# Optimization experiments

Hardware: AMD Instinct MI355X
Metric: run time of the kernel (lower is better)

Reference implementation:

```python
import jax, jax.numpy as jnp
import numpy as np

HEADS = 16
HEAD_DIM = 64
DIM = 1024
INNER = HEADS * HEAD_DIM
EPS = 1e-5


def setup_inputs() -> dict:
    key = jax.random.key(0)
    k_x, k_qkv, k_out, k_b = jax.random.split(key, 4)
    B, L = 2, 2048
    x = jax.random.normal(k_x, (B, L, DIM), dtype=jnp.float32)
    # Linear weights stored as [in, out] for x @ W
    w_qkv = jax.random.normal(k_qkv, (DIM, 3 * INNER), dtype=jnp.float32) * (DIM ** -0.5)
    w_out = jax.random.normal(k_out, (INNER, DIM), dtype=jnp.float32) * (INNER ** -0.5)
    b_out = jax.random.normal(k_b, (DIM,), dtype=jnp.float32) * 0.02
    gamma = jnp.ones((DIM,), dtype=jnp.float32)
    beta = jnp.zeros((DIM,), dtype=jnp.float32)
    return {"x": x, "w_qkv": w_qkv, "w_out": w_out, "b_out": b_out, "gamma": gamma, "beta": beta}


def reference(x, w_qkv, w_out, b_out, gamma, beta):
    B, L, C = x.shape
    scale = HEAD_DIM ** -0.5
    qkv = x @ w_qkv  # [B, L, 3*INNER]
    q, k, v = jnp.split(qkv, 3, axis=-1)
    # [B, L, INNER] -> [B, H, L, D]
    def split_heads(t):
        return t.reshape(B, L, HEADS, HEAD_DIM).transpose(0, 2, 1, 3)
    q, k, v = split_heads(q), split_heads(k), split_heads(v)
    dots = jnp.einsum('bhid,bhjd->bhij', q, k) * scale
    attn = jax.nn.softmax(dots, axis=-1)
    out = jnp.einsum('bhij,bhjd->bhid', attn, v)
    out = out.transpose(0, 2, 1, 3).reshape(B, L, INNER)
    out = out @ w_out + b_out
    res = x + out
    mean = jnp.mean(res, axis=-1, keepdims=True)
    var = jnp.var(res, axis=-1, keepdims=True)
    return (res - mean) * jax.lax.rsqrt(var + EPS) * gamma + beta
```

## Files before the change

kernel.cpp:

```cpp
#include <hip/hip_runtime.h>
#include <hip/hip_bf16.h>
#include <stdint.h>

#define HEADS 16
#define HDIM  64
#define DIMC  1024
#define INNER 1024
#define LSEQ  2048
#define BLM   4096

typedef unsigned short u16;
typedef __attribute__((ext_vector_type(8))) short bf16x8;
typedef __attribute__((ext_vector_type(4))) float f32x4;

__device__ __forceinline__ u16 f2bf(float f) {
  union { float f; uint32_t u; } v; v.f = f;
  uint32_t u = v.u;
  return (u16)((u + 0x7fffu + ((u >> 16) & 1u)) >> 16);
}
__device__ __forceinline__ uint32_t pack_bf2(float a, float b) {
  float2 f2; f2.x = a; f2.y = b;
  __hip_bfloat162 t = __float22bfloat162_rn(f2);
  union { __hip_bfloat162 h; uint32_t u; } c; c.h = t; return c.u;
}

__device__ __forceinline__ void load_lds16(const void* g, void* l) {
  __builtin_amdgcn_global_load_lds(
      (const __attribute__((address_space(1))) uint32_t*)g,
      (__attribute__((address_space(3))) uint32_t*)l, 16, 0, 0);
}

__global__ __launch_bounds__(256) void cast_bf16_k(const float* __restrict__ in,
                                                   u16* __restrict__ out, int n) {
  int i = (blockIdx.x * 256 + threadIdx.x) * 4;
  if (i < n) {
    float4 v = *(const float4*)(in + i);
    ushort4 o;
    o.x = f2bf(v.x); o.y = f2bf(v.y); o.z = f2bf(v.z); o.w = f2bf(v.w);
    *(ushort4*)(out + i) = o;
  }
}

__global__ __launch_bounds__(256) void transpose_cast_k(const float* __restrict__ in,
                                                        u16* __restrict__ out,
                                                        int R, int C) {
  __shared__ float tile[32][33];
  int c0 = blockIdx.x * 32, r0 = blockIdx.y * 32;
  int j = threadIdx.x & 31, i0 = threadIdx.x >> 5;
#pragma unroll
  for (int p = 0; p < 4; ++p) {
    int i = i0 + p * 8;
    tile[i][j] = in[(size_t)(r0 + i) * C + (c0 + j)];
  }
  __syncthreads();
#pragma unroll
  for (int p = 0; p < 4; ++p) {
    int i = i0 + p * 8;
    out[(size_t)(c0 + i) * R + (r0 + j)] = f2bf(tile[j][i]);
  }
}

template <int EPI>
__global__ __launch_bounds__(256) void gemm_bt(const u16* __restrict__ A,
                                               const u16* __restrict__ Bt,
                                               u16* __restrict__ Cb,
                                               float* __restrict__ Cf,
                                               const float* __restrict__ bias,
                                               const float* __restrict__ resid,
                                               u16* __restrict__ Vt,
                                               int M, int N, int K) {
  __shared__ alignas(16) u16 As[128 * 32];
  __shared__ alignas(16) u16 Bs[128 * 32];
  const int tid = threadIdx.x;
  const int lane = tid & 63;
  const int w = tid >> 6;
  const int wm = w >> 1, wn = w & 1;
  const int m0 = blockIdx.y * 128, n0 = blockIdx.x * 128;
  const int ln = lane & 15, qq = lane >> 4;
  const f32x4 zero4 = {0.f, 0.f, 0.f, 0.f};

  f32x4 acc[4][4];
#pragma unroll
  for (int i = 0; i < 4; ++i)
#pragma unroll
    for (int j = 0; j < 4; ++j) acc[i][j] = zero4;

  for (int kt = 0; kt < K; kt += 32) {
    __syncthreads();
#pragma unroll
    for (int iss = 0; iss < 2; ++iss) {
      int t = iss * 256 + tid;
      int r = t >> 2;
      int cl = (t & 3) ^ ((r >> 1) & 3);
      load_lds16(A + (size_t)(m0 + r) * K + kt + cl * 8,
                 (char*)As + (iss * 256 + w * 64) * 16);
      load_lds16(Bt + (size_t)(n0 + r) * K + kt + cl * 8,
                 (char*)Bs + (iss * 256 + w * 64) * 16);
    }
    __syncthreads();
    bf16x8 af[4], bfr[4];
#pragma unroll
    for (int i = 0; i < 4; ++i) {
      int ra = wm * 64 + i * 16 + ln;
      af[i] = *(const bf16x8*)(As + (ra * 4 + (qq ^ ((ra >> 1) & 3))) * 8);
      int rb = wn * 64 + i * 16 + ln;
      bfr[i] = *(const bf16x8*)(Bs + (rb * 4 + (qq ^ ((rb >> 1) & 3))) * 8);
    }
#pragma unroll
    for (int i = 0; i < 4; ++i)
#pragma unroll
      for (int j = 0; j < 4; ++j)
        acc[i][j] = __builtin_amdgcn_mfma_f32_16x16x32_bf16(af[i], bfr[j],
                                                            acc[i][j], 0, 0, 0);
  }

#pragma unroll
  for (int i = 0; i < 4; ++i) {
#pragma unroll
    for (int j = 0; j < 4; ++j) {
      int col = n0 + wn * 64 + j * 16 + ln;
      if (EPI == 0) {
#pragma unroll
        for (int rr = 0; rr < 4; ++rr) {
          int row = m0 + wm * 64 + i * 16 + qq * 4 + rr;
          Cb[(size_t)row * N + col] = f2bf(acc[i][j][rr]);
        }
      } else if (EPI == 1) {
#pragma unroll
        for (int rr = 0; rr < 4; ++rr) {
          int row = m0 + wm * 64 + i * 16 + qq * 4 + rr;
          Cf[(size_t)row * N + col] =
              acc[i][j][rr] + bias[col] + resid[(size_t)row * N + col];
        }
      } else {
        if (col < 2048) {
#pragma unroll
          for (int rr = 0; rr < 4; ++rr) {
            int row = m0 + wm * 64 + i * 16 + qq * 4 + rr;
            Cb[(size_t)row * 2048 + col] = f2bf(acc[i][j][rr]);
          }
        } else {
          int dg = col - 2048;
          int hh = dg >> 6, dd = dg & 63;
          int l0 = (m0 & 2047) + wm * 64 + i * 16 + qq * 4;
          int bb = m0 >> 11;
          ushort4 pk;
          pk.x = f2bf(acc[i][j][0]); pk.y = f2bf(acc[i][j][1]);
          pk.z = f2bf(acc[i][j][2]); pk.w = f2bf(acc[i][j][3]);
          *(ushort4*)(Vt + (((size_t)bb * 16 + hh) * 64 + dd) * 2048 + l0) = pk;
        }
      }
    }
  }
}

__global__ __launch_bounds__(256) void attn_fused(const u16* __restrict__ qk,
                                                  const u16* __restrict__ vt,
                                                  u16* __restrict__ outp) {
  const int qt = blockIdx.x & 31;
  const int h = (blockIdx.x >> 5) & 15;
  const int b = blockIdx.x >> 9;
  const int tid = threadIdx.x;
  const int lane = tid & 63;
  const int w = tid >> 6;
  const int ln = lane & 15, q4 = lane >> 4;
  const int l7 = ln & 7;
  const f32x4 zero4 = {0.f, 0.f, 0.f, 0.f};

  __shared__ alignas(16) u16 Ks[64 * 64];
  __shared__ alignas(16) u16 Vs[64 * 64];
  __shared__ alignas(16) u16 Ps[4][16 * 72];

  const size_t bh_tok = (size_t)b * LSEQ;
  const size_t vbase = ((size_t)b * 16 + h) * 64 * 2048;
  const int baseQ = h * HDIM;

  bf16x8 qf[2];
  {
    int row = qt * 64 + w * 16 + ln;
    const u16* p = qk + (bh_tok + row) * 2048 + baseQ;
#pragma unroll
    for (int ks = 0; ks < 2; ++ks) {
      bf16x8 v = *(const bf16x8*)(p + q4 * 8 + 32 * ks);
      bf16x8 o;
#pragma unroll
      for (int jj = 0; jj < 8; ++jj) {
        union { uint32_t u; float f; } cv; cv.u = ((uint32_t)(u16)v[jj]) << 16;
        o[jj] = (short)f2bf(cv.f * 0.125f);
      }
      qf[ks] = o;
    }
  }

  float mT = -1e30f, lsum = 0.f;
  f32x4 o_acc[4];
#pragma unroll
  for (int dt = 0; dt < 4; ++dt) o_acc[dt] = zero4;

  u16* pw_base = &Ps[w][0];

  for (int jt = 0; jt < 32; ++jt) {
    const int key0 = jt * 64;
    __syncthreads();
#pragma unroll
    for (int iss = 0; iss < 2; ++iss) {
      int idx = iss * 256 + tid;
      int row = idx >> 3, c = idx & 7;
      int cl = c ^ (row & 7);
      load_lds16(qk + (bh_tok + key0 + row) * 2048 + 1024 + baseQ + cl * 8,
                 (char*)Ks + (iss * 256 + w * 64) * 16);
      load_lds16(vt + vbase + (size_t)row * 2048 + key0 + cl * 8,
                 (char*)Vs + (iss * 256 + w * 64) * 16);
    }
    __syncthreads();

    f32x4 S[4];
#pragma unroll
    for (int kt = 0; kt < 4; ++kt) {
      f32x4 a = zero4;
#pragma unroll
      for (int ks = 0; ks < 2; ++ks) {
        bf16x8 kf = *(const bf16x8*)(
            Ks + (((kt * 16 + ln) * 8 + ((ks * 4 + q4) ^ l7)) * 8));
        a = __builtin_amdgcn_mfma_f32_16x16x32_bf16(kf, qf[ks], a, 0, 0, 0);
      }
      S[kt] = a;
    }

    float mx = S[0][0];
#pragma unroll
    for (int kt = 0; kt < 4; ++kt)
#pragma unroll
      for (int r = 0; r < 4; ++r) mx = fmaxf(mx, S[kt][r]);
    mx = fmaxf(mx, __shfl_xor(mx, 16));
    mx = fmaxf(mx, __shfl_xor(mx, 32));
    float mnew = fmaxf(mT, mx);
    float alpha = __expf(mT - mnew);
    float sl = 0.f;
#pragma unroll
    for (int kt = 0; kt < 4; ++kt)
#pragma unroll
      for (int r = 0; r < 4; ++r) {
        float p = __expf(S[kt][r] - mnew);
        S[kt][r] = p;
        sl += p;
      }
    sl += __shfl_xor(sl, 16);
    sl += __shfl_xor(sl, 32);
    lsum = lsum * alpha + sl;
    mT = mnew;
#pragma unroll
    for (int dt = 0; dt < 4; ++dt) o_acc[dt] *= alpha;

#pragma unroll
    for (int kt = 0; kt < 4; ++kt)
#pragma unroll
      for (int hh = 0; hh < 2; ++hh) {
        uint32_t pd = pack_bf2(S[kt][2 * hh], S[kt][2 * hh + 1]);
        *(uint32_t*)(pw_base + ln * 72 + kt * 16 + q4 * 4 + 2 * hh) = pd;
      }
    asm volatile("s_waitcnt lgkmcnt(0)" ::: "memory");

    bf16x8 pf0 = *(const bf16x8*)(pw_base + ln * 72 + 0 * 32 + q4 * 8);
    bf16x8 pf1 = *(const bf16x8*)(pw_base + ln * 72 + 1 * 32 + q4 * 8);

#pragma unroll
    for (int dt = 0; dt < 4; ++dt) {
      bf16x8 va0 = *(const bf16x8*)(
          Vs + (((dt * 16 + ln) * 8 + ((0 * 4 + q4) ^ l7)) * 8));
      o_acc[dt] = __builtin_amdgcn_mfma_f32_16x16x32_bf16(va0, pf0, o_acc[dt], 0, 0, 0);
      bf16x8 va1 = *(const bf16x8*)(
          Vs + (((dt * 16 + ln) * 8 + ((1 * 4 + q4) ^ l7)) * 8));
      o_acc[dt] = __builtin_amdgcn_mfma_f32_16x16x32_bf16(va1, pf1, o_acc[dt], 0, 0, 0);
    }
  }

  float rl = 1.0f / lsum;
  asm volatile("s_waitcnt lgkmcnt(0)" ::: "memory");
#pragma unroll
  for (int dt = 0; dt < 4; ++dt)
#pragma unroll
    for (int hh = 0; hh < 2; ++hh) {
      uint32_t pd = pack_bf2(o_acc[dt][2 * hh] * rl, o_acc[dt][2 * hh + 1] * rl);
      *(uint32_t*)(pw_base + ln * 72 + dt * 16 + q4 * 4 + 2 * hh) = pd;
    }
  asm volatile("s_waitcnt lgkmcnt(0)" ::: "memory");
#pragma unroll
  for (int half = 0; half < 2; ++half) {
    int rr = half * 8 + (lane >> 3);
    int ch = lane & 7;
    bf16x8 rowv = *(const bf16x8*)(pw_base + rr * 72 + ch * 8);
    int tok = qt * 64 + w * 16 + rr;
    *(bf16x8*)(outp + (bh_tok + tok) * 1024 + baseQ + ch * 8) = rowv;
  }
}

__global__ __launch_bounds__(256) void ln_k(const float* __restrict__ res,
                                            const float* __restrict__ gamma,
                                            const float* __restrict__ beta,
                                            float* __restrict__ out) {
  int row = blockIdx.x;
  const float* r = res + (size_t)row * DIMC;
  int tid = threadIdx.x;
  float4 v = *(const float4*)(r + tid * 4);
  float s = v.x + v.y + v.z + v.w;
  float ss = v.x * v.x + v.y * v.y + v.z * v.z + v.w * v.w;
#pragma unroll
  for (int off = 1; off < 64; off <<= 1) {
    s += __shfl_xor(s, off);
    ss += __shfl_xor(ss, off);
  }
  __shared__ float sbuf[8];
  int w = tid >> 6, lane = tid & 63;
  if (lane == 0) { sbuf[w] = s; sbuf[4 + w] = ss; }
  __syncthreads();
  s = sbuf[0] + sbuf[1] + sbuf[2] + sbuf[3];
  ss = sbuf[4] + sbuf[5] + sbuf[6] + sbuf[7];
  float mean = s * (1.0f / DIMC);
  float var = ss * (1.0f / DIMC) - mean * mean;
  float inv = rsqrtf(var + 1e-5f);
  float4 g = *(const float4*)(gamma + tid * 4);
  float4 bt = *(const float4*)(beta + tid * 4);
  float4 o;
  o.x = (v.x - mean) * inv * g.x + bt.x;
  o.y = (v.y - mean) * inv * g.y + bt.y;
  o.z = (v.z - mean) * inv * g.z + bt.z;
  o.w = (v.w - mean) * inv * g.w + bt.w;
  *(float4*)(out + (size_t)row * DIMC + tid * 4) = o;
}

extern "C" void kernel_launch(void* const* d_in, const int* in_sizes, int n_in,
                              void* d_out, int out_size, void* d_ws, size_t ws_size,
                              hipStream_t stream) {
  const float* x = (const float*)d_in[0];
  const float* w_qkv = (const float*)d_in[1];
  const float* w_out = (const float*)d_in[2];
  const float* b_out = (const float*)d_in[3];
  const float* gamma = (const float*)d_in[4];
  const float* beta = (const float*)d_in[5];
  float* outp = (float*)d_out;
  char* ws = (char*)d_ws;

  u16* xb = (u16*)(ws);
  u16* wqkvT = (u16*)(ws + ((size_t)8 << 20));
  u16* qk = (u16*)(ws + ((size_t)14 << 20));
  u16* vt = (u16*)(ws + ((size_t)30 << 20));
  u16* attnout = (u16*)(ws);
  u16* woutT = (u16*)(ws + ((size_t)8 << 20));
  float* res = (float*)(ws + ((size_t)14 << 20));

  cast_bf16_k<<<4096, 256, 0, stream>>>(x, xb, BLM * DIMC);
  transpose_cast_k<<<dim3(96, 32), 256, 0, stream>>>(w_qkv, wqkvT, 1024, 3072);
  gemm_bt<2><<<dim3(24, 32), 256, 0, stream>>>(xb, wqkvT, qk, nullptr, nullptr,
                                               nullptr, vt, BLM, 3072, 1024);
  transpose_cast_k<<<dim3(32, 32), 256, 0, stream>>>(w_out, woutT, 1024, 1024);
  attn_fused<<<1024, 256, 0, stream>>>(qk, vt, attnout);
  gemm_bt<1><<<dim3(8, 32), 256, 0, stream>>>(attnout, woutT, nullptr, res, b_out,
                                              x, nullptr, BLM, 1024, 1024);
  ln_k<<<4096, 256, 0, stream>>>(res, gamma, beta, outp);
}
```

Before: 231.3 us.

## Widen GEMM K-tile, shrink out-proj M-tile, use exp2 softmax, one-wave-per-row LayerNorm

The GEMM now loads 64-wide K slices per iteration with an 8-way XOR swizzle and is templated on M-tile size. The output projection uses 64-row tiles to double its block count and occupancy. Attention folds log2(e) into the Q scale so it can use exp2f, and it writes P/O fragments as 8-byte stores. LayerNorm assigns one wavefront per row, removing the shared-memory reduction and block barrier. The trade-offs are double the LDS use per GEMM block and a smaller tile that reuses less data.

```diff
diff --git a/kernel.cpp b/kernel.cpp
--- a/kernel.cpp
+++ b/kernel.cpp
@@ -60,7 +60,7 @@
   }
 }
 
-template <int EPI>
+template <int EPI, int TM>
 __global__ __launch_bounds__(256) void gemm_bt(const u16* __restrict__ A,
                                                const u16* __restrict__ Bt,
                                                u16* __restrict__ Cb,
@@ -69,66 +69,73 @@
                                                const float* __restrict__ resid,
                                                u16* __restrict__ Vt,
                                                int M, int N, int K) {
-  __shared__ alignas(16) u16 As[128 * 32];
-  __shared__ alignas(16) u16 Bs[128 * 32];
+  constexpr int MI = TM / 32;
+  __shared__ alignas(16) u16 As[TM * 64];
+  __shared__ alignas(16) u16 Bs[128 * 64];
   const int tid = threadIdx.x;
   const int lane = tid & 63;
   const int w = tid >> 6;
   const int wm = w >> 1, wn = w & 1;
-  const int m0 = blockIdx.y * 128, n0 = blockIdx.x * 128;
+  const int m0 = blockIdx.y * TM, n0 = blockIdx.x * 128;
   const int ln = lane & 15, qq = lane >> 4;
   const f32x4 zero4 = {0.f, 0.f, 0.f, 0.f};
 
-  f32x4 acc[4][4];
-#pragma unroll
-  for (int i = 0; i < 4; ++i)
+  f32x4 acc[MI][4];
+#pragma unroll
+  for (int i = 0; i < MI; ++i)
 #pragma unroll
     for (int j = 0; j < 4; ++j) acc[i][j] = zero4;
 
-  for (int kt = 0; kt < K; kt += 32) {
+  for (int kt = 0; kt < K; kt += 64) {
     __syncthreads();
 #pragma unroll
-    for (int iss = 0; iss < 2; ++iss) {
-      int t = iss * 256 + tid;
-      int r = t >> 2;
-      int cl = (t & 3) ^ ((r >> 1) & 3);
+    for (int p = 0; p < TM / 32; ++p) {
+      int t = p * 256 + tid;
+      int r = t >> 3;
+      int cl = (t & 7) ^ (r & 7);
       load_lds16(A + (size_t)(m0 + r) * K + kt + cl * 8,
-                 (char*)As + (iss * 256 + w * 64) * 16);
+                 (char*)As + (p * 256 + w * 64) * 16);
+    }
+#pragma unroll
+    for (int p = 0; p < 4; ++p) {
+      int t = p * 256 + tid;
+      int r = t >> 3;
+      int cl = (t & 7) ^ (r & 7);
       load_lds16(Bt + (size_t)(n0 + r) * K + kt + cl * 8,
-                 (char*)Bs + (iss * 256 + w * 64) * 16);
+                 (char*)Bs + (p * 256 + w * 64) * 16);
     }
     __syncthreads();
-    bf16x8 af[4], bfr[4];
-#pragma unroll
-    for (int i = 0; i < 4; ++i) {
-      int ra = wm * 64 + i * 16 + ln;
-      af[i] = *(const bf16x8*)(As + (ra * 4 + (qq ^ ((ra >> 1) & 3))) * 8);
-      int rb = wn * 64 + i * 16 + ln;
-      bfr[i] = *(const bf16x8*)(Bs + (rb * 4 + (qq ^ ((rb >> 1) & 3))) * 8);
-    }
-#pragma unroll
-    for (int i = 0; i < 4; ++i)
-#pragma unroll
-      for (int j = 0; j < 4; ++j)
-        acc[i][j] = __builtin_amdgcn_mfma_f32_16x16x32_bf16(af[i], bfr[j],
-                                                            acc[i][j], 0, 0, 0);
-  }
-
-#pragma unroll
-  for (int i = 0; i < 4; ++i) {
+#pragma unroll
+    for (int ks = 0; ks < 2; ++ks) {
+      bf16x8 af[MI], bfr[4];
+#pragma unroll
+      for (int i = 0; i < MI; ++i) {
+        int ra = wm * (TM / 2) + i * 16 + ln;
+        af[i] = *(const bf16x8*)(As + (ra * 8 + ((ks * 4 + qq) ^ (ra & 7))) * 8);
+      }
+#pragma unroll
+      for (int j = 0; j < 4; ++j) {
+        int rb = wn * 64 + j * 16 + ln;
+        bfr[j] = *(const bf16x8*)(Bs + (rb * 8 + ((ks * 4 + qq) ^ (rb & 7))) * 8);
+      }
+#pragma unroll
+      for (int i = 0; i < MI; ++i)
+#pragma unroll
+        for (int j = 0; j < 4; ++j)
+          acc[i][j] = __builtin_amdgcn_mfma_f32_16x16x32_bf16(af[i], bfr[j],
+                                                              acc[i][j], 0, 0, 0);
+    }
+  }
+
+#pragma unroll
+  for (int i = 0; i < MI; ++i) {
 #pragma unroll
     for (int j = 0; j < 4; ++j) {
       int col = n0 + wn * 64 + j * 16 + ln;
-      if (EPI == 0) {
+      if (EPI == 1) {
 #pragma unroll
         for (int rr = 0; rr < 4; ++rr) {
-          int row = m0 + wm * 64 + i * 16 + qq * 4 + rr;
-          Cb[(size_t)row * N + col] = f2bf(acc[i][j][rr]);
-        }
-      } else if (EPI == 1) {
-#pragma unroll
-        for (int rr = 0; rr < 4; ++rr) {
-          int row = m0 + wm * 64 + i * 16 + qq * 4 + rr;
+          int row = m0 + wm * (TM / 2) + i * 16 + qq * 4 + rr;
           Cf[(size_t)row * N + col] =
               acc[i][j][rr] + bias[col] + resid[(size_t)row * N + col];
         }
@@ -136,13 +143,13 @@
         if (col < 2048) {
 #pragma unroll
           for (int rr = 0; rr < 4; ++rr) {
-            int row = m0 + wm * 64 + i * 16 + qq * 4 + rr;
+            int row = m0 + wm * (TM / 2) + i * 16 + qq * 4 + rr;
             Cb[(size_t)row * 2048 + col] = f2bf(acc[i][j][rr]);
           }
         } else {
           int dg = col - 2048;
           int hh = dg >> 6, dd = dg & 63;
-          int l0 = (m0 & 2047) + wm * 64 + i * 16 + qq * 4;
+          int l0 = (m0 & 2047) + wm * (TM / 2) + i * 16 + qq * 4;
           int bb = m0 >> 11;
           ushort4 pk;
           pk.x = f2bf(acc[i][j][0]); pk.y = f2bf(acc[i][j][1]);
@@ -175,6 +182,7 @@
   const size_t vbase = ((size_t)b * 16 + h) * 64 * 2048;
   const int baseQ = h * HDIM;
 
+  const float qscale = 0.125f * 1.44269504088896340736f;
   bf16x8 qf[2];
   {
     int row = qt * 64 + w * 16 + ln;
@@ -186,7 +194,7 @@
 #pragma unroll
       for (int jj = 0; jj < 8; ++jj) {
         union { uint32_t u; float f; } cv; cv.u = ((uint32_t)(u16)v[jj]) << 16;
-        o[jj] = (short)f2bf(cv.f * 0.125f);
+        o[jj] = (short)f2bf(cv.f * qscale);
       }
       qf[ks] = o;
     }
@@ -235,13 +243,13 @@
     mx = fmaxf(mx, __shfl_xor(mx, 16));
     mx = fmaxf(mx, __shfl_xor(mx, 32));
     float mnew = fmaxf(mT, mx);
-    float alpha = __expf(mT - mnew);
+    float alpha = exp2f(mT - mnew);
     float sl = 0.f;
 #pragma unroll
     for (int kt = 0; kt < 4; ++kt)
 #pragma unroll
       for (int r = 0; r < 4; ++r) {
-        float p = __expf(S[kt][r] - mnew);
+        float p = exp2f(S[kt][r] - mnew);
         S[kt][r] = p;
         sl += p;
       }
@@ -253,12 +261,12 @@
     for (int dt = 0; dt < 4; ++dt) o_acc[dt] *= alpha;
 
 #pragma unroll
-    for (int kt = 0; kt < 4; ++kt)
-#pragma unroll
-      for (int hh = 0; hh < 2; ++hh) {
-        uint32_t pd = pack_bf2(S[kt][2 * hh], S[kt][2 * hh + 1]);
-        *(uint32_t*)(pw_base + ln * 72 + kt * 16 + q4 * 4 + 2 * hh) = pd;
-      }
+    for (int kt = 0; kt < 4; ++kt) {
+      uint2 pd;
+      pd.x = pack_bf2(S[kt][0], S[kt][1]);
+      pd.y = pack_bf2(S[kt][2], S[kt][3]);
+      *(uint2*)(pw_base + ln * 72 + kt * 16 + q4 * 4) = pd;
+    }
     asm volatile("s_waitcnt lgkmcnt(0)" ::: "memory");
 
     bf16x8 pf0 = *(const bf16x8*)(pw_base + ln * 72 + 0 * 32 + q4 * 8);
@@ -278,12 +286,12 @@
   float rl = 1.0f / lsum;
   asm volatile("s_waitcnt lgkmcnt(0)" ::: "memory");
 #pragma unroll
-  for (int dt = 0; dt < 4; ++dt)
-#pragma unroll
-    for (int hh = 0; hh < 2; ++hh) {
-      uint32_t pd = pack_bf2(o_acc[dt][2 * hh] * rl, o_acc[dt][2 * hh + 1] * rl);
-      *(uint32_t*)(pw_base + ln * 72 + dt * 16 + q4 * 4 + 2 * hh) = pd;
-    }
+  for (int dt = 0; dt < 4; ++dt) {
+    uint2 pd;
+    pd.x = pack_bf2(o_acc[dt][0] * rl, o_acc[dt][1] * rl);
+    pd.y = pack_bf2(o_acc[dt][2] * rl, o_acc[dt][3] * rl);
+    *(uint2*)(pw_base + ln * 72 + dt * 16 + q4 * 4) = pd;
+  }
   asm volatile("s_waitcnt lgkmcnt(0)" ::: "memory");
 #pragma unroll
   for (int half = 0; half < 2; ++half) {
@@ -299,34 +307,37 @@
                                             const float* __restrict__ gamma,
                                             const float* __restrict__ beta,
                                             float* __restrict__ out) {
-  int row = blockIdx.x;
+  int w = threadIdx.x >> 6, lane = threadIdx.x & 63;
+  int row = blockIdx.x * 4 + w;
   const float* r = res + (size_t)row * DIMC;
-  int tid = threadIdx.x;
-  float4 v = *(const float4*)(r + tid * 4);
-  float s = v.x + v.y + v.z + v.w;
-  float ss = v.x * v.x + v.y * v.y + v.z * v.z + v.w * v.w;
+  float4 v[4];
+  float s = 0.f, ss = 0.f;
+#pragma unroll
+  for (int p = 0; p < 4; ++p) {
+    v[p] = *(const float4*)(r + (p * 64 + lane) * 4);
+    s += v[p].x + v[p].y + v[p].z + v[p].w;
+    ss += v[p].x * v[p].x + v[p].y * v[p].y + v[p].z * v[p].z + v[p].w * v[p].w;
+  }
 #pragma unroll
   for (int off = 1; off < 64; off <<= 1) {
     s += __shfl_xor(s, off);
     ss += __shfl_xor(ss, off);
   }
-  __shared__ float sbuf[8];
-  int w = tid >> 6, lane = tid & 63;
-  if (lane == 0) { sbuf[w] = s; sbuf[4 + w] = ss; }
-  __syncthreads();
-  s = sbuf[0] + sbuf[1] + sbuf[2] + sbuf[3];
-  ss = sbuf[4] + sbuf[5] + sbuf[6] + sbuf[7];
   float mean = s * (1.0f / DIMC);
   float var = ss * (1.0f / DIMC) - mean * mean;
   float inv = rsqrtf(var + 1e-5f);
-  float4 g = *(const float4*)(gamma + tid * 4);
-  float4 bt = *(const float4*)(beta + tid * 4);
-  float4 o;
-  o.x = (v.x - mean) * inv * g.x + bt.x;
-  o.y = (v.y - mean) * inv * g.y + bt.y;
-  o.z = (v.z - mean) * inv * g.z + bt.z;
-  o.w = (v.w - mean) * inv * g.w + bt.w;
-  *(float4*)(out + (size_t)row * DIMC + tid * 4) = o;
+#pragma unroll
+  for (int p = 0; p < 4; ++p) {
+    int c = (p * 64 + lane) * 4;
+    float4 g = *(const float4*)(gamma + c);
+    float4 bt = *(const float4*)(beta + c);
+    float4 o;
+    o.x = (v[p].x - mean) * inv * g.x + bt.x;
+    o.y = (v[p].y - mean) * inv * g.y + bt.y;
+    o.z = (v[p].z - mean) * inv * g.z + bt.z;
+    o.w = (v[p].w - mean) * inv * g.w + bt.w;
+    *(float4*)(out + (size_t)row * DIMC + c) = o;
+  }
 }
 
 extern "C" void kernel_launch(void* const* d_in, const int* in_sizes, int n_in,
@@ -351,11 +362,13 @@
 
   cast_bf16_k<<<4096, 256, 0, stream>>>(x, xb, BLM * DIMC);
   transpose_cast_k<<<dim3(96, 32), 256, 0, stream>>>(w_qkv, wqkvT, 1024, 3072);
-  gemm_bt<2><<<dim3(24, 32), 256, 0, stream>>>(xb, wqkvT, qk, nullptr, nullptr,
-                                               nullptr, vt, BLM, 3072, 1024);
+  gemm_bt<2, 128><<<dim3(24, 32), 256, 0, stream>>>(xb, wqkvT, qk, nullptr,
+                                                    nullptr, nullptr, vt,
+                                                    BLM, 3072, 1024);
   transpose_cast_k<<<dim3(32, 32), 256, 0, stream>>>(w_out, woutT, 1024, 1024);
   attn_fused<<<1024, 256, 0, stream>>>(qk, vt, attnout);
-  gemm_bt<1><<<dim3(8, 32), 256, 0, stream>>>(attnout, woutT, nullptr, res, b_out,
-                                              x, nullptr, BLM, 1024, 1024);
-  ln_k<<<4096, 256, 0, stream>>>(res, gamma, beta, outp);
-}
+  gemm_bt<1, 64><<<dim3(8, 64), 256, 0, stream>>>(attnout, woutT, nullptr, res,
+                                                  b_out, x, nullptr,
+                                                  BLM, 1024, 1024);
+  ln_k<<<1024, 256, 0, stream>>>(res, gamma, beta, outp);
+}
```

After: 235.5 us. Within noise of the previous version (+1.8%).
